# Kernel tuning notes

Hardware: AMD Instinct MI355X
Metric: run time of the kernel (lower is better)

Reference implementation:

```python
import jax, jax.numpy as jnp
import numpy as np

B, T = 128, 50
VOCAB, EMB_D, GRU_H = 10000, 200, 100
HEADS, AHID, THID = 8, 96, 96

def _conv(x, w, b, pad):
    y = jax.lax.conv_general_dilated(x, w, (1, 1), pad,
        dimension_numbers=('NCHW', 'OIHW', 'NCHW'))
    return y + b[None, :, None, None]

def _bn(x, g, b, m, v):
    s = jax.lax.rsqrt(v + 1e-5)
    return (x - m[None, :, None, None]) * (g * s)[None, :, None, None] + b[None, :, None, None]

def _maxpool(x):
    return jax.lax.reduce_window(x, -jnp.inf, jax.lax.max, (1, 1, 2, 2), (1, 1, 2, 2), 'VALID')

def _resize(x):
    # F.interpolate(mode='bilinear', align_corners=False) == half-pixel bilinear, no antialias
    return jax.image.resize(x, (x.shape[0], x.shape[1], 25, 156), 'bilinear', antialias=False)

def _audio_attn(x, wq, bq, wk, bk, wv, bv):
    # x: [B,96,H,W]; wq: [heads,96,96] == stacked per-head 1x1 convs
    Q = jnp.einsum('bchw,noc->bnohw', x, wq) + bq[None, :, :, None, None]
    K = jnp.einsum('bchw,noc->bnohw', x, wk) + bk[None, :, :, None, None]
    V = jnp.einsum('bchw,noc->bnohw', x, wv) + bv[None, :, :, None, None]
    # torch F.softmax with no dim on a 4D tensor defaults to dim=1 (channels) -> axis=2 here
    return jax.nn.softmax(Q * K, axis=2) * V  # [B,heads,96,H,W]

def _text_attn(o, wq, bq, wk, bk, wv, bv):
    # o: [N,100]; wq: [heads,96,100] == stacked per-head Linear layers
    Q = jnp.einsum('nd,hod->nho', o, wq) + bq[None]
    K = jnp.einsum('nd,hod->nho', o, wk) + bk[None]
    V = jnp.einsum('nd,hod->nho', o, wv) + bv[None]
    a = jax.nn.softmax(Q * K, axis=2) * V  # 2D softmax default dim=1 -> over feature axis
    return a.reshape(o.shape[0], -1)  # head-concat order == torch cat along dim=1

def _gru(xs, w_ih, w_hh, b_ih, b_hh):
    # xs: [T,B,200]; torch gate order r, z, n; b_hn applied inside r-gating
    def step(h, x):
        gi = x @ w_ih.T + b_ih
        gh = h @ w_hh.T + b_hh
        ir, iz, inew = jnp.split(gi, 3, axis=1)
        hr, hz, hnew = jnp.split(gh, 3, axis=1)
        r = jax.nn.sigmoid(ir + hr)
        z = jax.nn.sigmoid(iz + hz)
        n = jnp.tanh(inew + r * hnew)
        h2 = (1.0 - z) * n + z * h
        return h2, h2
    h0 = jnp.zeros((xs.shape[1], GRU_H), xs.dtype)
    hT, outs = jax.lax.scan(step, h0, xs)
    return outs, hT

def _forward(tokens, lengths, mfcc_t, mfcc_f, mfcc_c, w1a, b1a, g1a, be1a, m1a, v1a, w1b, b1b, g1b, be1b, m1b, v1b, w2, b2, g2, be2, m2, v2, w3, b3, g3, be3, m3, v3, w4, b4, g4, be4, m4, v4, wq_a1, bq_a1, wk_a1, bk_a1, wv_a1, bv_a1, wq_a2, bq_a2, wk_a2, bk_a2, wv_a2, bv_a2, emb, w_ih, w_hh, b_ih, b_hh, wq_t1, bq_t1, wk_t1, bk_t1, wv_t1, bv_t1, wq_t2, bq_t2, wk_t2, bk_t2, wv_t2, bv_t2, w_fa, b_fa, w_ft, b_ft, w_e, b_e):
    # --- audio CNN stem (eval-mode batchnorm; dropout off) ---
    xa = jax.nn.relu(_bn(_conv(mfcc_t, w1a, b1a, 'VALID'), g1a, be1a, m1a, v1a))
    xb = jax.nn.relu(_bn(_conv(mfcc_f, w1b, b1b, 'VALID'), g1b, be1b, m1b, v1b))
    # NOTE: original source reuses conv1b/bn1b for the third input (faithful to that)
    xc = jax.nn.relu(_bn(_conv(mfcc_c, w1b, b1b, 'VALID'), g1b, be1b, m1b, v1b))
    x = jnp.concatenate([_resize(xa), _resize(xb), _resize(xc)], axis=1)  # [B,24,25,156]
    x = _maxpool(jax.nn.relu(_bn(_conv(x, w2, b2, [(1, 1), (1, 1)]), g2, be2, m2, v2)))  # [B,32,12,78]
    x = _maxpool(jax.nn.relu(_bn(_conv(x, w3, b3, [(1, 1), (1, 1)]), g3, be3, m3, v3)))  # [B,64,6,39]
    x = jax.nn.relu(_bn(_conv(x, w4, b4, [(1, 1), (1, 1)]), g4, be4, m4, v4))            # [B,96,6,39]
    # --- two stacked per-head audio attentions, then per-head spatial GAP ---
    a1 = _audio_attn(x, wq_a1, bq_a1, wk_a1, bk_a1, wv_a1, bv_a1).mean(axis=(-2, -1))  # [B,8,96]
    a2 = _audio_attn(x, wq_a2, bq_a2, wk_a2, bk_a2, wv_a2, bv_a2).mean(axis=(-2, -1))
    # forward() slices heads along the height concat and GAPs -> per head [stage1 96, stage2 96]
    self_attn_audio = jnp.concatenate([a1, a2], axis=2).reshape(x.shape[0], -1)  # [B,1536]
    # --- text branch: embedding + GRU (all lengths == T -> pack/pad is identity) ---
    ex = jnp.swapaxes(emb[tokens], 0, 1)  # [T,B,200]
    outs, h = _gru(ex, w_ih, w_hh, b_ih, b_hh)  # h: [B,100]
    output = jnp.swapaxes(outs, 0, 1).reshape(-1, GRU_H)  # [B*T,100]
    t1 = _text_attn(output, wq_t1, bq_t1, wk_t1, bk_t1, wv_t1, bv_t1)
    t2 = _text_attn(output, wq_t2, bq_t2, wk_t2, bk_t2, wv_t2, bv_t2)
    self_attn_text = jnp.concatenate([t1, t2], axis=1).reshape(x.shape[0], T, -1).sum(axis=1)  # [B,1536]
    # --- cross-modal gated fusion ---
    x_gap = x.mean(axis=(-2, -1))  # [B,96]
    a_text = jax.nn.softmax(x_gap @ w_fa.T + b_fa, axis=1)   # [B,100]
    attn_text_based_audio = a_text * h                        # [B,100]
    a_audio = jax.nn.softmax(h @ w_ft.T + b_ft, axis=1)      # [B,96]
    attn_audio_based_text = a_audio * x_gap                   # [B,96]
    feat = jnp.concatenate([self_attn_audio, self_attn_text,
                            attn_audio_based_text, attn_text_based_audio], axis=1)  # [B,3268]
    return feat @ w_e.T + b_e  # [B,4] emotion logits

def setup_inputs() -> dict:
    key = jax.random.key(0)
    ks = iter(jax.random.split(key, 100))
    nrm = lambda s, sc=0.05: jax.random.normal(next(ks), s, jnp.float32) * sc
    uni = lambda s: jax.random.uniform(next(ks), s, jnp.float32) * 0.5 + 0.5
    d = {}
    d['mfcc_t'] = jax.random.normal(next(ks), (B, 1, 200, 40), jnp.float32)
    d['mfcc_f'] = jax.random.normal(next(ks), (B, 1, 200, 40), jnp.float32)
    d['mfcc_c'] = jax.random.normal(next(ks), (B, 1, 200, 40), jnp.float32)
    d['tokens'] = jax.random.randint(next(ks), (B, T), 0, VOCAB)
    d['lengths'] = jnp.full((B,), T, jnp.int32)
    def bnp(pre, c):
        d['g' + pre] = 1.0 + nrm((c,)); d['be' + pre] = nrm((c,))
        d['m' + pre] = nrm((c,)); d['v' + pre] = uni((c,))
    d['w1a'] = nrm((8, 1, 5, 2), 0.2); d['b1a'] = nrm((8,)); bnp('1a', 8)
    d['w1b'] = nrm((8, 1, 2, 6), 0.2); d['b1b'] = nrm((8,)); bnp('1b', 8)
    d['w2'] = nrm((32, 24, 3, 3), 0.1); d['b2'] = nrm((32,)); bnp('2', 32)
    d['w3'] = nrm((64, 32, 3, 3), 0.1); d['b3'] = nrm((64,)); bnp('3', 64)
    d['w4'] = nrm((96, 64, 3, 3), 0.08); d['b4'] = nrm((96,)); bnp('4', 96)
    for s in ('1', '2'):
        for p in ('q', 'k', 'v'):
            d['w%s_a%s' % (p, s)] = nrm((HEADS, 96, 96), 0.1)
            d['b%s_a%s' % (p, s)] = nrm((HEADS, 96))
    d['emb'] = nrm((VOCAB, EMB_D), 0.1)
    d['w_ih'] = nrm((3 * GRU_H, EMB_D), 0.1); d['w_hh'] = nrm((3 * GRU_H, GRU_H), 0.1)
    d['b_ih'] = nrm((3 * GRU_H,)); d['b_hh'] = nrm((3 * GRU_H,))
    for s in ('1', '2'):
        for p in ('q', 'k', 'v'):
            d['w%s_t%s' % (p, s)] = nrm((HEADS, THID, GRU_H), 0.1)
            d['b%s_t%s' % (p, s)] = nrm((HEADS, THID))
    d['w_fa'] = nrm((100, 96), 0.1); d['b_fa'] = nrm((100,))
    d['w_ft'] = nrm((96, 100), 0.1); d['b_ft'] = nrm((96,))
    d['w_e'] = nrm((4, 2 * HEADS * AHID + 2 * HEADS * THID + 96 + 100), 0.05); d['b_e'] = nrm((4,))
    return d

def reference(mfcc_t, mfcc_f, mfcc_c, tokens, lengths, w1a, b1a, g1a, be1a, m1a, v1a, w1b, b1b, g1b, be1b, m1b, v1b, w2, b2, g2, be2, m2, v2, w3, b3, g3, be3, m3, v3, w4, b4, g4, be4, m4, v4, wq_a1, bq_a1, wk_a1, bk_a1, wv_a1, bv_a1, wq_a2, bq_a2, wk_a2, bk_a2, wv_a2, bv_a2, emb, w_ih, w_hh, b_ih, b_hh, wq_t1, bq_t1, wk_t1, bk_t1, wv_t1, bv_t1, wq_t2, bq_t2, wk_t2, bk_t2, wv_t2, bv_t2, w_fa, b_fa, w_ft, b_ft, w_e, b_e):
    return _forward(tokens, lengths, mfcc_t, mfcc_f, mfcc_c, w1a, b1a, g1a, be1a, m1a, v1a, w1b, b1b, g1b, be1b, m1b, v1b, w2, b2, g2, be2, m2, v2, w3, b3, g3, be3, m3, v3, w4, b4, g4, be4, m4, v4, wq_a1, bq_a1, wk_a1, bk_a1, wv_a1, bv_a1, wq_a2, bq_a2, wk_a2, bk_a2, wv_a2, bv_a2, emb, w_ih, w_hh, b_ih, b_hh, wq_t1, bq_t1, wk_t1, bk_t1, wv_t1, bv_t1, wq_t2, bq_t2, wk_t2, bk_t2, wv_t2, bv_t2, w_fa, b_fa, w_ft, b_ft, w_e, b_e)
```

## Files before the change

kernel.cpp:

```cpp
#include <hip/hip_runtime.h>
#include <math.h>

static constexpr int kB = 128;
static constexpr int kT = 50;

struct TDesc { const float* src; float* dst; int O; int C; int total; };
struct TPack { TDesc d[15]; };
__global__ void k_transpose_pack(TPack p, float* __restrict__ za) {
    if (blockIdx.y == 15) {
        for (int i = blockIdx.x * 256 + threadIdx.x; i < 196608; i += 76800)
            za[i] = 0.f;
        return;
    }
    TDesc t = p.d[blockIdx.y];
    int idx = blockIdx.x * 256 + threadIdx.x;
    if (idx >= t.total) return;
    int o = idx % t.O; int r = idx / t.O; int c = r % t.C; int n = r / t.C;
    t.dst[idx] = t.src[((size_t)n * t.O + o) * t.C + c];
}

__global__ void __launch_bounds__(320) k_gi(const int* __restrict__ tokens,
        const float* __restrict__ emb, const float* __restrict__ w_ih,
        const float* __restrict__ b_ih, float* __restrict__ GI) {
    int r0 = blockIdx.x * 8;
    int tid = threadIdx.x;
    __shared__ float er[8][200];
    for (int e = tid; e < 1600; e += 320) {
        int r = e / 200, c = e - r * 200;
        er[r][c] = emb[(size_t)tokens[r0 + r] * 200 + c];
    }
    __syncthreads();
    if (tid < 300) {
        float acc[8];
        float bv = b_ih[tid];
        #pragma unroll
        for (int r = 0; r < 8; ++r) acc[r] = bv;
        for (int k4 = 0; k4 < 50; ++k4) {
            float4 w4 = *(const float4*)(w_ih + (size_t)tid * 200 + k4 * 4);
            #pragma unroll
            for (int r = 0; r < 8; ++r) {
                float4 x4 = *(const float4*)&er[r][k4 * 4];
                acc[r] += w4.x * x4.x + w4.y * x4.y + w4.z * x4.z + w4.w * x4.w;
            }
        }
        #pragma unroll
        for (int r = 0; r < 8; ++r)
            GI[(size_t)(r0 + r) * 300 + tid] = acc[r];
    }
}

__global__ void __launch_bounds__(256) k_fat_stem_gru(
    const float* __restrict__ mt, const float* __restrict__ mf,
    const float* __restrict__ mc,
    const float* __restrict__ w1a, const float* __restrict__ b1a,
    const float* __restrict__ g1a, const float* __restrict__ be1a,
    const float* __restrict__ m1a, const float* __restrict__ v1a,
    const float* __restrict__ w1b, const float* __restrict__ b1b,
    const float* __restrict__ g1b, const float* __restrict__ be1b,
    const float* __restrict__ m1b, const float* __restrict__ v1b,
    float* __restrict__ out, int total,
    const float* __restrict__ GI, const float* __restrict__ w_hh,
    const float* __restrict__ b_hh, float* __restrict__ outs) {
    if (blockIdx.x < 128) {
        const int b = blockIdx.x, tid = threadIdx.x;
        __shared__ float hs[100];
        __shared__ float gH[300];
        const float bias0 = b_hh[tid];
        const float bias1 = (tid < 44) ? b_hh[256 + tid] : 0.f;
        if (tid < 100) hs[tid] = 0.f;
        __syncthreads();
        for (int t = 0; t < kT; ++t) {
            {
                float gh = bias0;
                const float* wr = w_hh + (size_t)tid * 100;
                #pragma unroll
                for (int k4 = 0; k4 < 25; ++k4) {
                    float4 w4 = *(const float4*)(wr + k4 * 4);
                    float4 h4 = *(const float4*)&hs[k4 * 4];
                    gh += w4.x * h4.x + w4.y * h4.y + w4.z * h4.z + w4.w * h4.w;
                }
                gH[tid] = gh;
            }
            if (tid < 44) {
                float gh = bias1;
                const float* wr = w_hh + (size_t)(256 + tid) * 100;
                #pragma unroll
                for (int k4 = 0; k4 < 25; ++k4) {
                    float4 w4 = *(const float4*)(wr + k4 * 4);
                    float4 h4 = *(const float4*)&hs[k4 * 4];
                    gh += w4.x * h4.x + w4.y * h4.y + w4.z * h4.z + w4.w * h4.w;
                }
                gH[256 + tid] = gh;
            }
            __syncthreads();
            if (tid < 100) {
                const float* gi = GI + ((size_t)b * kT + t) * 300;
                float r = 1.f / (1.f + expf(-(gi[tid] + gH[tid])));
                float z = 1.f / (1.f + expf(-(gi[100 + tid] + gH[100 + tid])));
                float nn = tanhf(gi[200 + tid] + r * gH[200 + tid]);
                float h2 = (1.f - z) * nn + z * hs[tid];
                hs[tid] = h2;
                outs[((size_t)b * kT + t) * 100 + tid] = h2;
            }
            __syncthreads();
        }
        return;
    }
    int idx = (blockIdx.x - 128) * 256 + threadIdx.x;
    if (idx >= total) return;
    int ox = idx % 156; int t = idx / 156;
    int oy = t % 25; t /= 25;
    int ch = t % 24; int b = t / 24;
    int grp = ch >> 3, c = ch & 7;
    const float* src; int Hc, Wc;
    const float *wb, *cb, *g, *be, *m, *v;
    if (grp == 0) { src = mt; Hc = 196; Wc = 39; wb = w1a + c * 10;
                    cb = b1a; g = g1a; be = be1a; m = m1a; v = v1a; }
    else          { src = (grp == 1 ? mf : mc); Hc = 199; Wc = 35; wb = w1b + c * 12;
                    cb = b1b; g = g1b; be = be1b; m = m1b; v = v1b; }
    float s = g[c] * rsqrtf(v[c] + 1e-5f);
    float bias = (cb[c] - m[c]) * s + be[c];
    float sy = (oy + 0.5f) * ((float)Hc / 25.f) - 0.5f;
    float sx = (ox + 0.5f) * ((float)Wc / 156.f) - 0.5f;
    float fy0 = floorf(sy), fx0 = floorf(sx);
    float fy = sy - fy0, fx = sx - fx0;
    int y0 = (int)fy0, x0 = (int)fx0;
    int y0c = min(max(y0, 0), Hc - 1), y1c = min(max(y0 + 1, 0), Hc - 1);
    int x0c = min(max(x0, 0), Wc - 1), x1c = min(max(x0 + 1, 0), Wc - 1);
    bool xs = (x1c == x0c), ys = (y1c == y0c);
    const float* p = src + (size_t)b * 8000;
    float t00, t01, t10, t11;
    if (grp == 0) {
        float W[6][3];
        #pragma unroll
        for (int r = 0; r < 6; ++r) {
            int rr = min(y0c + r, 199);
            #pragma unroll
            for (int cc = 0; cc < 3; ++cc)
                W[r][cc] = p[rr * 40 + min(x0c + cc, 39)];
        }
        float a00 = 0.f, a01 = 0.f, a10 = 0.f, a11 = 0.f;
        #pragma unroll
        for (int ky = 0; ky < 5; ++ky)
            #pragma unroll
            for (int kx = 0; kx < 2; ++kx) {
                float wv = wb[ky * 2 + kx];
                a00 += W[ky][kx] * wv;     a01 += W[ky][kx + 1] * wv;
                a10 += W[ky + 1][kx] * wv; a11 += W[ky + 1][kx + 1] * wv;
            }
        t00 = a00;
        t01 = xs ? a00 : a01;
        t10 = ys ? a00 : a10;
        t11 = xs ? (ys ? a00 : a10) : (ys ? a01 : a11);
    } else {
        float W[3][7];
        #pragma unroll
        for (int r = 0; r < 3; ++r) {
            int rr = min(y0c + r, 199);
            #pragma unroll
            for (int cc = 0; cc < 7; ++cc)
                W[r][cc] = p[rr * 40 + min(x0c + cc, 39)];
        }
        float a00 = 0.f, a01 = 0.f, a10 = 0.f, a11 = 0.f;
        #pragma unroll
        for (int ky = 0; ky < 2; ++ky)
            #pragma unroll
            for (int kx = 0; kx < 6; ++kx) {
                float wv = wb[ky * 6 + kx];
                a00 += W[ky][kx] * wv;     a01 += W[ky][kx + 1] * wv;
                a10 += W[ky + 1][kx] * wv; a11 += W[ky + 1][kx + 1] * wv;
            }
        t00 = a00;
        t01 = xs ? a00 : a01;
        t10 = ys ? a00 : a10;
        t11 = xs ? (ys ? a00 : a10) : (ys ? a01 : a11);
    }
    float r00 = fmaxf(t00 * s + bias, 0.f), r01 = fmaxf(t01 * s + bias, 0.f);
    float r10 = fmaxf(t10 * s + bias, 0.f), r11 = fmaxf(t11 * s + bias, 0.f);
    out[idx] = r00 * (1.f - fy) * (1.f - fx) + r01 * (1.f - fy) * fx
             + r10 * fy * (1.f - fx) + r11 * fy * fx;
}

template<int CIN, int CI_T, int H, int W, int ROWS, int NPX>
__global__ void __launch_bounds__(256) k_conv3x3_tiled(
    const float* __restrict__ in, const float* __restrict__ wT,
    const float* __restrict__ cb, const float* __restrict__ g,
    const float* __restrict__ be, const float* __restrict__ m,
    const float* __restrict__ v, float* __restrict__ out, int COUT) {
    constexpr int WP = W + 2;
    constexpr int RP = ROWS + 2;
    constexpr int STAGE = CI_T * RP * WP;
    __shared__ float sx[STAGE];
    __shared__ float sw[CI_T * 9 * 8];
    const int b = blockIdx.x, rt = blockIdx.y, oc0 = blockIdx.z * 8;
    const int row0 = rt * ROWS;
    const int tid = threadIdx.x;

    int off[NPX]; bool val[NPX];
    #pragma unroll
    for (int j = 0; j < NPX; ++j) {
        int px = tid + j * 256;
        int oy = px / W, ox = px - oy * W;
        bool ok = (px < ROWS * W) && (row0 + oy < H);
        val[j] = ok;
        off[j] = ok ? (oy * WP + ox) : 0;
    }

    float acc[NPX][8];
    #pragma unroll
    for (int j = 0; j < NPX; ++j)
        #pragma unroll
        for (int o = 0; o < 8; ++o) acc[j][o] = 0.f;

    for (int c0 = 0; c0 < CIN; c0 += CI_T) {
        __syncthreads();
        for (int e = tid; e < STAGE; e += 256) {
            int ci = e / (RP * WP);
            int rem = e - ci * RP * WP;
            int r = rem / WP;
            int xx = rem - r * WP;
            int iy = row0 - 1 + r;
            int ix = xx - 1;
            float vv = 0.f;
            if (iy >= 0 && iy < H && ix >= 0 && ix < W)
                vv = in[((size_t)(b * CIN + c0 + ci) * H + iy) * W + ix];
            sx[e] = vv;
        }
        for (int e = tid; e < CI_T * 9 * 8; e += 256) {
            int rk = e >> 3;
            int o = e & 7;
            sw[e] = wT[((size_t)c0 * 9 + rk) * COUT + oc0 + o];
        }
        __syncthreads();
        #pragma unroll 1
        for (int cl = 0; cl < CI_T; ++cl) {
            const float* sxc = sx + cl * RP * WP;
            #pragma unroll
            for (int k = 0; k < 9; ++k) {
                const int ky = k / 3, kx = k % 3;
                const float4 wa = *(const float4*)(sw + (cl * 9 + k) * 8);
                const float4 wb = *(const float4*)(sw + (cl * 9 + k) * 8 + 4);
                #pragma unroll
                for (int j = 0; j < NPX; ++j) {
                    float xv = sxc[off[j] + ky * WP + kx];
                    acc[j][0] += xv * wa.x; acc[j][1] += xv * wa.y;
                    acc[j][2] += xv * wa.z; acc[j][3] += xv * wa.w;
                    acc[j][4] += xv * wb.x; acc[j][5] += xv * wb.y;
                    acc[j][6] += xv * wb.z; acc[j][7] += xv * wb.w;
                }
            }
        }
    }
    float sc[8], bi[8];
    #pragma unroll
    for (int o = 0; o < 8; ++o) {
        float s = g[oc0 + o] * rsqrtf(v[oc0 + o] + 1e-5f);
        sc[o] = s; bi[o] = (cb[oc0 + o] - m[oc0 + o]) * s + be[oc0 + o];
    }
    #pragma unroll
    for (int j = 0; j < NPX; ++j) if (val[j]) {
        int px = tid + j * 256;
        int oy = row0 + px / W, ox = px % W;
        #pragma unroll
        for (int o = 0; o < 8; ++o)
            out[((size_t)(b * COUT + oc0 + o) * H + oy) * W + ox] =
                fmaxf(acc[j][o] * sc[o] + bi[o], 0.f);
    }
}

__global__ void k_maxpool(const float* __restrict__ in, float* __restrict__ out,
                          int C, int Hin, int Win, int Hout, int Wout, int total) {
    int idx = blockIdx.x * blockDim.x + threadIdx.x;
    if (idx >= total) return;
    int ox = idx % Wout; int t = idx / Wout;
    int oy = t % Hout; t /= Hout;
    int c = t % C; int b = t / C;
    const float* p = in + ((size_t)(b * C + c) * Hin + 2 * oy) * Win + 2 * ox;
    float m0 = fmaxf(p[0], p[1]);
    float m1 = fmaxf(p[Win], p[Win + 1]);
    out[idx] = fmaxf(m0, m1);
}

__global__ void __launch_bounds__(256) k_xgap(const float* __restrict__ x,
                                              float* __restrict__ xgap) {
    int b = blockIdx.x, tid = threadIdx.x;
    int wave = tid >> 6, lane = tid & 63;
    for (int c = wave; c < 96; c += 4) {
        const float* row = x + ((size_t)b * 96 + c) * 234;
        float s = 0.f;
        for (int p = lane; p < 234; p += 64) s += row[p];
        #pragma unroll
        for (int off = 1; off < 64; off <<= 1) s += __shfl_xor(s, off);
        if (lane == 0) xgap[b * 96 + c] = s * (1.f / 234.f);
    }
}

__global__ void __launch_bounds__(256, 2) k_audio_attn(
    const float* __restrict__ x,
    const float* __restrict__ wq1, const float* __restrict__ bq1,
    const float* __restrict__ wk1, const float* __restrict__ bk1,
    const float* __restrict__ wv1, const float* __restrict__ bv1,
    const float* __restrict__ wq2, const float* __restrict__ bq2,
    const float* __restrict__ wk2, const float* __restrict__ bk2,
    const float* __restrict__ wv2, const float* __restrict__ bv2,
    float* __restrict__ afeat) {
    const int b = blockIdx.x >> 1, pt = blockIdx.x & 1;
    const int n = blockIdx.y, stage = blockIdx.z;
    const float* wq = (stage ? wq2 : wq1) + n * 9216;
    const float* wk = (stage ? wk2 : wk1) + n * 9216;
    const float* wv = (stage ? wv2 : wv1) + n * 9216;
    const float* bqn = (stage ? bq2 : bq1) + n * 96;
    const float* bkn = (stage ? bk2 : bk1) + n * 96;
    const float* bvn = (stage ? bv2 : bv1) + n * 96;
    const int tid = threadIdx.x;
    const int to = tid >> 4, tpg = tid & 15;
    const int ob = to * 6;
    const int pA = tpg * 4;
    const int p0 = pt * 128;

    __shared__ float sxc[16 * 128];
    __shared__ float sw[4608];
    float* sred = sw;

    const float* xb = x + (size_t)b * (96 * 234) + p0;

    float qa[6][8], ka[6][8], va[6][8];
    #pragma unroll
    for (int j = 0; j < 6; ++j) {
        float bq_ = bqn[ob + j], bk_ = bkn[ob + j], bv_ = bvn[ob + j];
        #pragma unroll
        for (int i = 0; i < 8; ++i) { qa[j][i] = bq_; ka[j][i] = bk_; va[j][i] = bv_; }
    }

    for (int c0 = 0; c0 < 96; c0 += 16) {
        __syncthreads();
        {
            #pragma unroll
            for (int it = 0; it < 4; ++it) {
                int e2 = tid + it * 256;
                int r = e2 >> 6, c2 = (e2 & 63) * 2;
                float2 v = make_float2(0.f, 0.f);
                if (p0 + c2 < 234) v = *(const float2*)(xb + (c0 + r) * 234 + c2);
                *(float2*)(sxc + r * 128 + c2) = v;
            }
        }
        for (int e4 = tid; e4 < 1152; e4 += 256) {
            int mat = (e4 >= 768) ? 2 : (e4 >= 384 ? 1 : 0);
            int r4 = e4 - mat * 384;
            const float* wsrc = (mat == 0) ? wq : (mat == 1 ? wk : wv);
            *(float4*)(sw + mat * 1536 + r4 * 4) = *(const float4*)(wsrc + c0 * 96 + r4 * 4);
        }
        __syncthreads();
        #pragma unroll 2
        for (int cc = 0; cc < 16; ++cc) {
            float4 xa = *(const float4*)(sxc + cc * 128 + pA);
            float4 xc = *(const float4*)(sxc + cc * 128 + 64 + pA);
            const float* wr = sw + cc * 96 + ob;
            float2 q01 = *(const float2*)(wr);
            float2 q23 = *(const float2*)(wr + 2);
            float2 q45 = *(const float2*)(wr + 4);
            float2 k01 = *(const float2*)(wr + 1536);
            float2 k23 = *(const float2*)(wr + 1538);
            float2 k45 = *(const float2*)(wr + 1540);
            float2 v01 = *(const float2*)(wr + 3072);
            float2 v23 = *(const float2*)(wr + 3074);
            float2 v45 = *(const float2*)(wr + 3076);
            float wqv[6] = {q01.x, q01.y, q23.x, q23.y, q45.x, q45.y};
            float wkv[6] = {k01.x, k01.y, k23.x, k23.y, k45.x, k45.y};
            float wvv[6] = {v01.x, v01.y, v23.x, v23.y, v45.x, v45.y};
            #pragma unroll
            for (int j = 0; j < 6; ++j) {
                qa[j][0] += wqv[j] * xa.x; qa[j][1] += wqv[j] * xa.y;
                qa[j][2] += wqv[j] * xa.z; qa[j][3] += wqv[j] * xa.w;
                qa[j][4] += wqv[j] * xc.x; qa[j][5] += wqv[j] * xc.y;
                qa[j][6] += wqv[j] * xc.z; qa[j][7] += wqv[j] * xc.w;
                ka[j][0] += wkv[j] * xa.x; ka[j][1] += wkv[j] * xa.y;
                ka[j][2] += wkv[j] * xa.z; ka[j][3] += wkv[j] * xa.w;
                ka[j][4] += wkv[j] * xc.x; ka[j][5] += wkv[j] * xc.y;
                ka[j][6] += wkv[j] * xc.z; ka[j][7] += wkv[j] * xc.w;
                va[j][0] += wvv[j] * xa.x; va[j][1] += wvv[j] * xa.y;
                va[j][2] += wvv[j] * xa.z; va[j][3] += wvv[j] * xa.w;
                va[j][4] += wvv[j] * xc.x; va[j][5] += wvv[j] * xc.y;
                va[j][6] += wvv[j] * xc.z; va[j][7] += wvv[j] * xc.w;
            }
        }
    }

    int col[8];
    #pragma unroll
    for (int i = 0; i < 4; ++i) { col[i] = pA + i; col[4 + i] = 64 + pA + i; }

    float pmx[8];
    #pragma unroll
    for (int i = 0; i < 8; ++i) pmx[i] = -1e30f;
    #pragma unroll
    for (int j = 0; j < 6; ++j)
        #pragma unroll
        for (int i = 0; i < 8; ++i) {
            float sv = qa[j][i] * ka[j][i];
            qa[j][i] = sv;
            pmx[i] = fmaxf(pmx[i], sv);
        }
    __syncthreads();
    #pragma unroll
    for (int i = 0; i < 8; ++i) sred[to * 128 + col[i]] = pmx[i];
    __syncthreads();
    float m_[8];
    #pragma unroll
    for (int i = 0; i < 8; ++i) {
        float mm = -1e30f;
        for (int t = 0; t < 16; ++t) mm = fmaxf(mm, sred[t * 128 + col[i]]);
        m_[i] = mm;
    }
    __syncthreads();
    float z[8];
    #pragma unroll
    for (int i = 0; i < 8; ++i) z[i] = 0.f;
    #pragma unroll
    for (int j = 0; j < 6; ++j)
        #pragma unroll
        for (int i = 0; i < 8; ++i) {
            float e = __expf(qa[j][i] - m_[i]);
            qa[j][i] = e;
            z[i] += e;
        }
    #pragma unroll
    for (int i = 0; i < 8; ++i) sred[to * 128 + col[i]] = z[i];
    __syncthreads();
    float rz[8];
    #pragma unroll
    for (int i = 0; i < 8; ++i) {
        float zs = 0.f;
        for (int t = 0; t < 16; ++t) zs += sred[t * 128 + col[i]];
        rz[i] = (p0 + col[i] < 234) ? 1.f / zs : 0.f;
    }
    __syncthreads();
    #pragma unroll
    for (int j = 0; j < 6; ++j) {
        float po = 0.f;
        #pragma unroll
        for (int i = 0; i < 8; ++i) po += qa[j][i] * rz[i] * va[j][i];
        sred[(ob + j) * 16 + tpg] = po;
    }
    __syncthreads();
    if (tid < 96) {
        float ssum = 0.f;
        #pragma unroll
        for (int t = 0; t < 16; ++t) ssum += sred[tid * 16 + t];
        atomicAdd(afeat + b * 1536 + n * 192 + stage * 96 + tid, ssum * (1.f / 234.f));
    }
}

__global__ void __launch_bounds__(128) k_text_attn(const float* __restrict__ outs,
    const float* __restrict__ wq1, const float* __restrict__ bq1,
    const float* __restrict__ wk1, const float* __restrict__ bk1,
    const float* __restrict__ wv1, const float* __restrict__ bv1,
    const float* __restrict__ wq2, const float* __restrict__ bq2,
    const float* __restrict__ wk2, const float* __restrict__ bk2,
    const float* __restrict__ wv2, const float* __restrict__ bv2,
    float* __restrict__ tfeat) {
    int b = blockIdx.x, stage = blockIdx.y, n = blockIdx.z;
    const float* wq = stage ? wq2 : wq1; const float* bq = stage ? bq2 : bq1;
    const float* wk = stage ? wk2 : wk1; const float* bk = stage ? bk2 : bk1;
    const float* wv = stage ? wv2 : wv1; const float* bv = stage ? bv2 : bv1;
    int tid = threadIdx.x;
    bool act = tid < 96;
    int oo = act ? tid : 0;
    const float* wqc = wq + n * 9600 + oo;
    const float* wkc = wk + n * 9600 + oo;
    const float* wvc = wv + n * 9600 + oo;
    float bqv = act ? bq[n * 96 + tid] : 0.f;
    float bkv = act ? bk[n * 96 + tid] : 0.f;
    float bvv = act ? bv[n * 96 + tid] : 0.f;
    __shared__ float rows[10][100];
    __shared__ float wredM[2][10], wredS[2][10];
    float acc = 0.f;
    int wave = tid >> 6, lane = tid & 63;
    for (int tile = 0; tile < 5; ++tile) {
        int t0 = tile * 10;
        __syncthreads();
        for (int e = tid; e < 1000; e += 128) {
            int tt = e / 100, c = e - tt * 100;
            rows[tt][c] = outs[((size_t)b * kT + t0 + tt) * 100 + c];
        }
        __syncthreads();
        float q[10], k[10], v[10];
        #pragma unroll
        for (int tt = 0; tt < 10; ++tt) { q[tt] = bqv; k[tt] = bkv; v[tt] = bvv; }
        for (int c4 = 0; c4 < 25; ++c4) {
            int cb = c4 * 4 * 96;
            float q0 = wqc[cb], q1 = wqc[cb + 96], q2 = wqc[cb + 192], q3 = wqc[cb + 288];
            float k0 = wkc[cb], k1 = wkc[cb + 96], k2 = wkc[cb + 192], k3 = wkc[cb + 288];
            float v0 = wvc[cb], v1 = wvc[cb + 96], v2 = wvc[cb + 192], v3 = wvc[cb + 288];
            #pragma unroll
            for (int tt = 0; tt < 10; ++tt) {
                float4 x4 = *(const float4*)&rows[tt][c4 * 4];
                q[tt] += q0 * x4.x + q1 * x4.y + q2 * x4.z + q3 * x4.w;
                k[tt] += k0 * x4.x + k1 * x4.y + k2 * x4.z + k3 * x4.w;
                v[tt] += v0 * x4.x + v1 * x4.y + v2 * x4.z + v3 * x4.w;
            }
        }
        float s[10], e_[10];
        #pragma unroll
        for (int tt = 0; tt < 10; ++tt) s[tt] = act ? q[tt] * k[tt] : -1e30f;
        #pragma unroll
        for (int tt = 0; tt < 10; ++tt) {
            float m = s[tt];
            #pragma unroll
            for (int off = 1; off < 64; off <<= 1) m = fmaxf(m, __shfl_xor(m, off));
            if (lane == 0) wredM[wave][tt] = m;
        }
        __syncthreads();
        #pragma unroll
        for (int tt = 0; tt < 10; ++tt) {
            float mx = fmaxf(wredM[0][tt], wredM[1][tt]);
            e_[tt] = expf(s[tt] - mx);
        }
        #pragma unroll
        for (int tt = 0; tt < 10; ++tt) {
            float sm = e_[tt];
            #pragma unroll
            for (int off = 1; off < 64; off <<= 1) sm += __shfl_xor(sm, off);
            if (lane == 0) wredS[wave][tt] = sm;
        }
        __syncthreads();
        #pragma unroll
        for (int tt = 0; tt < 10; ++tt) {
            float sm = wredS[0][tt] + wredS[1][tt];
            acc += e_[tt] / sm * v[tt];
        }
    }
    if (act) tfeat[b * 1536 + stage * 768 + n * 96 + tid] = acc;
}

__global__ void __launch_bounds__(128) k_final(const float* __restrict__ xgap,
    const float* __restrict__ outs, const float* __restrict__ afeat,
    const float* __restrict__ tfeat,
    const float* __restrict__ w_fa, const float* __restrict__ b_fa,
    const float* __restrict__ w_ft, const float* __restrict__ b_ft,
    const float* __restrict__ w_e, const float* __restrict__ b_e,
    float* __restrict__ out) {
    int b = blockIdx.x; int tid = threadIdx.x;
    __shared__ float xg[96], hv[100], st[100], sa[96], aat[96], atba[100];
    __shared__ float redm[2], reds[2];
    if (tid < 96) xg[tid] = xgap[b * 96 + tid];
    if (tid < 100) hv[tid] = outs[(size_t)(b * kT + kT - 1) * 100 + tid];
    __syncthreads();
    if (tid < 100) {
        float acc = b_fa[tid];
        const float* wr = w_fa + tid * 96;
        for (int c = 0; c < 96; ++c) acc += wr[c] * xg[c];
        st[tid] = acc;
    }
    if (tid < 96) {
        float acc = b_ft[tid];
        const float* wr = w_ft + tid * 100;
        for (int c = 0; c < 100; ++c) acc += wr[c] * hv[c];
        sa[tid] = acc;
    }
    __syncthreads();
    if (tid == 0) {
        float mxv = -1e30f; for (int i = 0; i < 100; ++i) mxv = fmaxf(mxv, st[i]);
        float s = 0.f; for (int i = 0; i < 100; ++i) s += expf(st[i] - mxv);
        redm[0] = mxv; reds[0] = s;
    }
    if (tid == 1) {
        float mxv = -1e30f; for (int i = 0; i < 96; ++i) mxv = fmaxf(mxv, sa[i]);
        float s = 0.f; for (int i = 0; i < 96; ++i) s += expf(sa[i] - mxv);
        redm[1] = mxv; reds[1] = s;
    }
    __syncthreads();
    if (tid < 100) atba[tid] = expf(st[tid] - redm[0]) / reds[0] * hv[tid];
    if (tid < 96)  aat[tid]  = expf(sa[tid] - redm[1]) / reds[1] * xg[tid];
    __syncthreads();
    float a0 = 0.f, a1 = 0.f, a2 = 0.f, a3 = 0.f;
    for (int col = tid; col < 3268; col += 128) {
        float f;
        if (col < 1536)      f = afeat[b * 1536 + col];
        else if (col < 3072) f = tfeat[b * 1536 + col - 1536];
        else if (col < 3168) f = aat[col - 3072];
        else                 f = atba[col - 3168];
        a0 += w_e[col] * f;            a1 += w_e[3268 + col] * f;
        a2 += w_e[2 * 3268 + col] * f; a3 += w_e[3 * 3268 + col] * f;
    }
    __shared__ float r4[4][128];
    r4[0][tid] = a0; r4[1][tid] = a1; r4[2][tid] = a2; r4[3][tid] = a3;
    __syncthreads();
    if (tid < 4) {
        float s = 0.f;
        for (int i = 0; i < 128; ++i) s += r4[tid][i];
        out[b * 4 + tid] = s + b_e[tid];
    }
}

extern "C" void kernel_launch(void* const* d_in, const int* in_sizes, int n_in,
                              void* d_out, int out_size, void* d_ws, size_t ws_size,
                              hipStream_t stream) {
    (void)in_sizes; (void)n_in; (void)out_size; (void)ws_size;
    const float* mfcc_t = (const float*)d_in[0];
    const float* mfcc_f = (const float*)d_in[1];
    const float* mfcc_c = (const float*)d_in[2];
    const int*   tokens = (const int*)d_in[3];
    const float *w1a = (const float*)d_in[5],  *b1a = (const float*)d_in[6],
                *g1a = (const float*)d_in[7],  *be1a = (const float*)d_in[8],
                *m1a = (const float*)d_in[9],  *v1a = (const float*)d_in[10];
    const float *w1b = (const float*)d_in[11], *b1b = (const float*)d_in[12],
                *g1b = (const float*)d_in[13], *be1b = (const float*)d_in[14],
                *m1b = (const float*)d_in[15], *v1b = (const float*)d_in[16];
    const float *w2 = (const float*)d_in[17], *b2 = (const float*)d_in[18],
                *g2 = (const float*)d_in[19], *be2 = (const float*)d_in[20],
                *m2 = (const float*)d_in[21], *v2 = (const float*)d_in[22];
    const float *w3 = (const float*)d_in[23], *b3 = (const float*)d_in[24],
                *g3 = (const float*)d_in[25], *be3 = (const float*)d_in[26],
                *m3 = (const float*)d_in[27], *v3 = (const float*)d_in[28];
    const float *w4 = (const float*)d_in[29], *b4 = (const float*)d_in[30],
                *g4 = (const float*)d_in[31], *be4 = (const float*)d_in[32],
                *m4 = (const float*)d_in[33], *v4 = (const float*)d_in[34];
    const float *wq_a1 = (const float*)d_in[35], *bq_a1 = (const float*)d_in[36],
                *wk_a1 = (const float*)d_in[37], *bk_a1 = (const float*)d_in[38],
                *wv_a1 = (const float*)d_in[39], *bv_a1 = (const float*)d_in[40];
    const float *wq_a2 = (const float*)d_in[41], *bq_a2 = (const float*)d_in[42],
                *wk_a2 = (const float*)d_in[43], *bk_a2 = (const float*)d_in[44],
                *wv_a2 = (const float*)d_in[45], *bv_a2 = (const float*)d_in[46];
    const float *emb  = (const float*)d_in[47];
    const float *w_ih = (const float*)d_in[48], *w_hh = (const float*)d_in[49],
                *b_ih = (const float*)d_in[50], *b_hh = (const float*)d_in[51];
    const float *wq_t1 = (const float*)d_in[52], *bq_t1 = (const float*)d_in[53],
                *wk_t1 = (const float*)d_in[54], *bk_t1 = (const float*)d_in[55],
                *wv_t1 = (const float*)d_in[56], *bv_t1 = (const float*)d_in[57];
    const float *wq_t2 = (const float*)d_in[58], *bq_t2 = (const float*)d_in[59],
                *wk_t2 = (const float*)d_in[60], *bk_t2 = (const float*)d_in[61],
                *wv_t2 = (const float*)d_in[62], *bv_t2 = (const float*)d_in[63];
    const float *w_fa = (const float*)d_in[64], *b_fa = (const float*)d_in[65],
                *w_ft = (const float*)d_in[66], *b_ft = (const float*)d_in[67],
                *w_e  = (const float*)d_in[68], *b_e  = (const float*)d_in[69];

    float* ws = (float*)d_ws;
    const size_t Z0 = 0;
    const size_t Z1 = 22091776ull;
    const size_t OUTS  = 34072576ull;
    const size_t AFEAT = 34712576ull;
    const size_t TFEAT = 34909184ull;
    const size_t XGAP  = 35105792ull;
    const size_t WT    = 35118080ull;
    float* GI = ws + Z0;
    float* X1 = ws + Z1;
    float* C2 = ws + Z0;  float* P2 = ws + Z1;
    float* C3 = ws + Z0;  float* P3 = ws + Z1;
    float* X4 = ws + Z0;
    float* outs  = ws + OUTS;
    float* afeat = ws + AFEAT;
    float* tfeat = ws + TFEAT;
    float* xgap  = ws + XGAP;
    float* wqa1t = ws + WT;
    float* wka1t = wqa1t + 73728; float* wva1t = wka1t + 73728;
    float* wqa2t = wva1t + 73728; float* wka2t = wqa2t + 73728; float* wva2t = wka2t + 73728;
    float* wqt1t = wva2t + 73728;
    float* wkt1t = wqt1t + 76800; float* wvt1t = wkt1t + 76800;
    float* wqt2t = wvt1t + 76800; float* wkt2t = wqt2t + 76800; float* wvt2t = wkt2t + 76800;
    float* wT2 = tfeat;
    float* wT3 = tfeat + 6912;
    float* wT4 = tfeat + 25344;

    TPack tp;
    tp.d[0]  = {wq_a1, wqa1t, 96, 96, 73728};
    tp.d[1]  = {wk_a1, wka1t, 96, 96, 73728};
    tp.d[2]  = {wv_a1, wva1t, 96, 96, 73728};
    tp.d[3]  = {wq_a2, wqa2t, 96, 96, 73728};
    tp.d[4]  = {wk_a2, wka2t, 96, 96, 73728};
    tp.d[5]  = {wv_a2, wva2t, 96, 96, 73728};
    tp.d[6]  = {w2, wT2, 32, 216, 6912};
    tp.d[7]  = {w3, wT3, 64, 288, 18432};
    tp.d[8]  = {w4, wT4, 96, 576, 55296};
    tp.d[9]  = {wq_t1, wqt1t, 96, 100, 76800};
    tp.d[10] = {wk_t1, wkt1t, 96, 100, 76800};
    tp.d[11] = {wv_t1, wvt1t, 96, 100, 76800};
    tp.d[12] = {wq_t2, wqt2t, 96, 100, 76800};
    tp.d[13] = {wk_t2, wkt2t, 96, 100, 76800};
    tp.d[14] = {wv_t2, wvt2t, 96, 100, 76800};
    k_transpose_pack<<<dim3(300, 16), 256, 0, stream>>>(tp, afeat);

    k_gi<<<kB * kT / 8, 320, 0, stream>>>(tokens, emb, w_ih, b_ih, GI);

    k_fat_stem_gru<<<46928, 256, 0, stream>>>(mfcc_t, mfcc_f, mfcc_c,
        w1a, b1a, g1a, be1a, m1a, v1a,
        w1b, b1b, g1b, be1b, m1b, v1b, X1, 11980800,
        GI, w_hh, b_hh, outs);

    k_conv3x3_tiled<24, 8, 25, 156, 9, 6><<<dim3(128, 3, 4), 256, 0, stream>>>(
        X1, wT2, b2, g2, be2, m2, v2, C2, 32);
    k_maxpool<<<14976, 256, 0, stream>>>(C2, P2, 32, 25, 156, 12, 78, 3833856);
    k_conv3x3_tiled<32, 8, 12, 78, 12, 4><<<dim3(128, 1, 8), 256, 0, stream>>>(
        P2, wT3, b3, g3, be3, m3, v3, C3, 64);
    k_maxpool<<<7488, 256, 0, stream>>>(C3, P3, 64, 12, 78, 6, 39, 1916928);
    k_conv3x3_tiled<64, 16, 6, 39, 6, 1><<<dim3(128, 1, 12), 256, 0, stream>>>(
        P3, wT4, b4, g4, be4, m4, v4, X4, 96);

    k_text_attn<<<dim3(kB, 2, 8), 128, 0, stream>>>(outs,
        wqt1t, bq_t1, wkt1t, bk_t1, wvt1t, bv_t1,
        wqt2t, bq_t2, wkt2t, bk_t2, wvt2t, bv_t2, tfeat);
    k_xgap<<<kB, 256, 0, stream>>>(X4, xgap);

    k_audio_attn<<<dim3(kB * 2, 8, 2), 256, 0, stream>>>(X4,
        wqa1t, bq_a1, wka1t, bk_a1, wva1t, bv_a1,
        wqa2t, bq_a2, wka2t, bk_a2, wva2t, bv_a2, afeat);

    k_final<<<kB, 128, 0, stream>>>(xgap, outs, afeat, tfeat,
                                    w_fa, b_fa, w_ft, b_ft, w_e, b_e, (float*)d_out);
}
```

Baseline: 1.419 ms.

## Retile text attention with register-blocked QKV projection and transposed GRU output

```diff
diff --git a/kernel.cpp b/kernel.cpp
--- a/kernel.cpp
+++ b/kernel.cpp
@@ -60,7 +60,7 @@
     const float* __restrict__ m1b, const float* __restrict__ v1b,
     float* __restrict__ out, int total,
     const float* __restrict__ GI, const float* __restrict__ w_hh,
-    const float* __restrict__ b_hh, float* __restrict__ outs) {
+    const float* __restrict__ b_hh, float* __restrict__ outsT) {
     if (blockIdx.x < 128) {
         const int b = blockIdx.x, tid = threadIdx.x;
         __shared__ float hs[100];
@@ -100,7 +100,7 @@
                 float nn = tanhf(gi[200 + tid] + r * gH[200 + tid]);
                 float h2 = (1.f - z) * nn + z * hs[tid];
                 hs[tid] = h2;
-                outs[((size_t)b * kT + t) * 100 + tid] = h2;
+                outsT[((size_t)b * 100 + tid) * kT + t] = h2;
             }
             __syncthreads();
         }
@@ -451,7 +451,8 @@
     }
 }
 
-__global__ void __launch_bounds__(128) k_text_attn(const float* __restrict__ outs,
+__global__ void __launch_bounds__(256, 2) k_text_attn(
+    const float* __restrict__ outsT,
     const float* __restrict__ wq1, const float* __restrict__ bq1,
     const float* __restrict__ wk1, const float* __restrict__ bk1,
     const float* __restrict__ wv1, const float* __restrict__ bv1,
@@ -459,82 +460,133 @@
     const float* __restrict__ wk2, const float* __restrict__ bk2,
     const float* __restrict__ wv2, const float* __restrict__ bv2,
     float* __restrict__ tfeat) {
-    int b = blockIdx.x, stage = blockIdx.y, n = blockIdx.z;
-    const float* wq = stage ? wq2 : wq1; const float* bq = stage ? bq2 : bq1;
-    const float* wk = stage ? wk2 : wk1; const float* bk = stage ? bk2 : bk1;
-    const float* wv = stage ? wv2 : wv1; const float* bv = stage ? bv2 : bv1;
-    int tid = threadIdx.x;
-    bool act = tid < 96;
-    int oo = act ? tid : 0;
-    const float* wqc = wq + n * 9600 + oo;
-    const float* wkc = wk + n * 9600 + oo;
-    const float* wvc = wv + n * 9600 + oo;
-    float bqv = act ? bq[n * 96 + tid] : 0.f;
-    float bkv = act ? bk[n * 96 + tid] : 0.f;
-    float bvv = act ? bv[n * 96 + tid] : 0.f;
-    __shared__ float rows[10][100];
-    __shared__ float wredM[2][10], wredS[2][10];
-    float acc = 0.f;
-    int wave = tid >> 6, lane = tid & 63;
-    for (int tile = 0; tile < 5; ++tile) {
-        int t0 = tile * 10;
+    const int b = blockIdx.x, stage = blockIdx.y, n = blockIdx.z;
+    const float* wq = (stage ? wq2 : wq1) + n * 9600;
+    const float* wk = (stage ? wk2 : wk1) + n * 9600;
+    const float* wv = (stage ? wv2 : wv1) + n * 9600;
+    const float* bqn = (stage ? bq2 : bq1) + n * 96;
+    const float* bkn = (stage ? bk2 : bk1) + n * 96;
+    const float* bvn = (stage ? bv2 : bv1) + n * 96;
+    const int tid = threadIdx.x;
+    const int to = tid >> 4, tpg = tid & 15;
+    const int ob = to * 6;
+    const int tA = tpg * 4;
+
+    __shared__ float sxc[20 * 64];
+    __shared__ float sw[5760];
+    float* sred = sw;
+
+    const float* xb = outsT + (size_t)b * (100 * kT);
+
+    float qa[6][4], ka[6][4], va[6][4];
+    #pragma unroll
+    for (int j = 0; j < 6; ++j) {
+        float bq_ = bqn[ob + j], bk_ = bkn[ob + j], bv_ = bvn[ob + j];
+        #pragma unroll
+        for (int i = 0; i < 4; ++i) { qa[j][i] = bq_; ka[j][i] = bk_; va[j][i] = bv_; }
+    }
+
+    for (int c0 = 0; c0 < 100; c0 += 20) {
         __syncthreads();
-        for (int e = tid; e < 1000; e += 128) {
-            int tt = e / 100, c = e - tt * 100;
-            rows[tt][c] = outs[((size_t)b * kT + t0 + tt) * 100 + c];
+        for (int e = tid; e < 1280; e += 256) {
+            int r = e >> 6, tt = e & 63;
+            sxc[e] = (tt < kT) ? xb[(c0 + r) * kT + tt] : 0.f;
+        }
+        for (int e4 = tid; e4 < 1440; e4 += 256) {
+            int mat = (e4 >= 960) ? 2 : (e4 >= 480 ? 1 : 0);
+            int r4 = e4 - mat * 480;
+            const float* wsrc = (mat == 0) ? wq : (mat == 1 ? wk : wv);
+            *(float4*)(sw + mat * 1920 + r4 * 4) = *(const float4*)(wsrc + c0 * 96 + r4 * 4);
         }
         __syncthreads();
-        float q[10], k[10], v[10];
-        #pragma unroll
-        for (int tt = 0; tt < 10; ++tt) { q[tt] = bqv; k[tt] = bkv; v[tt] = bvv; }
-        for (int c4 = 0; c4 < 25; ++c4) {
-            int cb = c4 * 4 * 96;
-            float q0 = wqc[cb], q1 = wqc[cb + 96], q2 = wqc[cb + 192], q3 = wqc[cb + 288];
-            float k0 = wkc[cb], k1 = wkc[cb + 96], k2 = wkc[cb + 192], k3 = wkc[cb + 288];
-            float v0 = wvc[cb], v1 = wvc[cb + 96], v2 = wvc[cb + 192], v3 = wvc[cb + 288];
-            #pragma unroll
-            for (int tt = 0; tt < 10; ++tt) {
-                float4 x4 = *(const float4*)&rows[tt][c4 * 4];
-                q[tt] += q0 * x4.x + q1 * x4.y + q2 * x4.z + q3 * x4.w;
-                k[tt] += k0 * x4.x + k1 * x4.y + k2 * x4.z + k3 * x4.w;
-                v[tt] += v0 * x4.x + v1 * x4.y + v2 * x4.z + v3 * x4.w;
-            }
-        }
-        float s[10], e_[10];
-        #pragma unroll
-        for (int tt = 0; tt < 10; ++tt) s[tt] = act ? q[tt] * k[tt] : -1e30f;
-        #pragma unroll
-        for (int tt = 0; tt < 10; ++tt) {
-            float m = s[tt];
-            #pragma unroll
-            for (int off = 1; off < 64; off <<= 1) m = fmaxf(m, __shfl_xor(m, off));
-            if (lane == 0) wredM[wave][tt] = m;
-        }
-        __syncthreads();
-        #pragma unroll
-        for (int tt = 0; tt < 10; ++tt) {
-            float mx = fmaxf(wredM[0][tt], wredM[1][tt]);
-            e_[tt] = expf(s[tt] - mx);
-        }
-        #pragma unroll
-        for (int tt = 0; tt < 10; ++tt) {
-            float sm = e_[tt];
-            #pragma unroll
-            for (int off = 1; off < 64; off <<= 1) sm += __shfl_xor(sm, off);
-            if (lane == 0) wredS[wave][tt] = sm;
-        }
-        __syncthreads();
-        #pragma unroll
-        for (int tt = 0; tt < 10; ++tt) {
-            float sm = wredS[0][tt] + wredS[1][tt];
-            acc += e_[tt] / sm * v[tt];
-        }
-    }
-    if (act) tfeat[b * 1536 + stage * 768 + n * 96 + tid] = acc;
+        #pragma unroll 4
+        for (int cc = 0; cc < 20; ++cc) {
+            float4 xa = *(const float4*)(sxc + cc * 64 + tA);
+            const float* wr = sw + cc * 96 + ob;
+            float2 q01 = *(const float2*)(wr);
+            float2 q23 = *(const float2*)(wr + 2);
+            float2 q45 = *(const float2*)(wr + 4);
+            float2 k01 = *(const float2*)(wr + 1920);
+            float2 k23 = *(const float2*)(wr + 1922);
+            float2 k45 = *(const float2*)(wr + 1924);
+            float2 v01 = *(const float2*)(wr + 3840);
+            float2 v23 = *(const float2*)(wr + 3842);
+            float2 v45 = *(const float2*)(wr + 3844);
+            float wqv[6] = {q01.x, q01.y, q23.x, q23.y, q45.x, q45.y};
+            float wkv[6] = {k01.x, k01.y, k23.x, k23.y, k45.x, k45.y};
+            float wvv[6] = {v01.x, v01.y, v23.x, v23.y, v45.x, v45.y};
+            #pragma unroll
+            for (int j = 0; j < 6; ++j) {
+                qa[j][0] += wqv[j] * xa.x; qa[j][1] += wqv[j] * xa.y;
+                qa[j][2] += wqv[j] * xa.z; qa[j][3] += wqv[j] * xa.w;
+                ka[j][0] += wkv[j] * xa.x; ka[j][1] += wkv[j] * xa.y;
+                ka[j][2] += wkv[j] * xa.z; ka[j][3] += wkv[j] * xa.w;
+                va[j][0] += wvv[j] * xa.x; va[j][1] += wvv[j] * xa.y;
+                va[j][2] += wvv[j] * xa.z; va[j][3] += wvv[j] * xa.w;
+            }
+        }
+    }
+
+    float pmx[4] = {-1e30f, -1e30f, -1e30f, -1e30f};
+    #pragma unroll
+    for (int j = 0; j < 6; ++j)
+        #pragma unroll
+        for (int i = 0; i < 4; ++i) {
+            float sv = qa[j][i] * ka[j][i];
+            qa[j][i] = sv;
+            pmx[i] = fmaxf(pmx[i], sv);
+        }
+    __syncthreads();
+    #pragma unroll
+    for (int i = 0; i < 4; ++i) sred[to * 64 + tA + i] = pmx[i];
+    __syncthreads();
+    float m_[4];
+    #pragma unroll
+    for (int i = 0; i < 4; ++i) {
+        float mm = -1e30f;
+        for (int t = 0; t < 16; ++t) mm = fmaxf(mm, sred[t * 64 + tA + i]);
+        m_[i] = mm;
+    }
+    __syncthreads();
+    float z[4] = {0.f, 0.f, 0.f, 0.f};
+    #pragma unroll
+    for (int j = 0; j < 6; ++j)
+        #pragma unroll
+        for (int i = 0; i < 4; ++i) {
+            float e = __expf(qa[j][i] - m_[i]);
+            qa[j][i] = e;
+            z[i] += e;
+        }
+    #pragma unroll
+    for (int i = 0; i < 4; ++i) sred[to * 64 + tA + i] = z[i];
+    __syncthreads();
+    float rz[4];
+    #pragma unroll
+    for (int i = 0; i < 4; ++i) {
+        float zs = 0.f;
+        for (int t = 0; t < 16; ++t) zs += sred[t * 64 + tA + i];
+        rz[i] = (tA + i < kT) ? 1.f / zs : 0.f;
+    }
+    __syncthreads();
+    #pragma unroll
+    for (int j = 0; j < 6; ++j) {
+        float po = qa[j][0] * rz[0] * va[j][0]
+                 + qa[j][1] * rz[1] * va[j][1]
+                 + qa[j][2] * rz[2] * va[j][2]
+                 + qa[j][3] * rz[3] * va[j][3];
+        sred[(ob + j) * 16 + tpg] = po;
+    }
+    __syncthreads();
+    if (tid < 96) {
+        float ssum = 0.f;
+        #pragma unroll
+        for (int t = 0; t < 16; ++t) ssum += sred[tid * 16 + t];
+        tfeat[b * 1536 + stage * 768 + n * 96 + tid] = ssum;
+    }
 }
 
 __global__ void __launch_bounds__(128) k_final(const float* __restrict__ xgap,
-    const float* __restrict__ outs, const float* __restrict__ afeat,
+    const float* __restrict__ outsT, const float* __restrict__ afeat,
     const float* __restrict__ tfeat,
     const float* __restrict__ w_fa, const float* __restrict__ b_fa,
     const float* __restrict__ w_ft, const float* __restrict__ b_ft,
@@ -544,7 +596,7 @@
     __shared__ float xg[96], hv[100], st[100], sa[96], aat[96], atba[100];
     __shared__ float redm[2], reds[2];
     if (tid < 96) xg[tid] = xgap[b * 96 + tid];
-    if (tid < 100) hv[tid] = outs[(size_t)(b * kT + kT - 1) * 100 + tid];
+    if (tid < 100) hv[tid] = outsT[((size_t)b * 100 + tid) * kT + (kT - 1)];
     __syncthreads();
     if (tid < 100) {
         float acc = b_fa[tid];
@@ -648,7 +700,7 @@
     float* C2 = ws + Z0;  float* P2 = ws + Z1;
     float* C3 = ws + Z0;  float* P3 = ws + Z1;
     float* X4 = ws + Z0;
-    float* outs  = ws + OUTS;
+    float* outsT = ws + OUTS;
     float* afeat = ws + AFEAT;
     float* tfeat = ws + TFEAT;
     float* xgap  = ws + XGAP;
@@ -685,7 +737,7 @@
     k_fat_stem_gru<<<46928, 256, 0, stream>>>(mfcc_t, mfcc_f, mfcc_c,
         w1a, b1a, g1a, be1a, m1a, v1a,
         w1b, b1b, g1b, be1b, m1b, v1b, X1, 11980800,
-        GI, w_hh, b_hh, outs);
+        GI, w_hh, b_hh, outsT);
 
     k_conv3x3_tiled<24, 8, 25, 156, 9, 6><<<dim3(128, 3, 4), 256, 0, stream>>>(
         X1, wT2, b2, g2, be2, m2, v2, C2, 32);
@@ -696,7 +748,7 @@
     k_conv3x3_tiled<64, 16, 6, 39, 6, 1><<<dim3(128, 1, 12), 256, 0, stream>>>(
         P3, wT4, b4, g4, be4, m4, v4, X4, 96);
 
-    k_text_attn<<<dim3(kB, 2, 8), 128, 0, stream>>>(outs,
+    k_text_attn<<<dim3(kB, 2, 8), 256, 0, stream>>>(outsT,
         wqt1t, bq_t1, wkt1t, bk_t1, wvt1t, bv_t1,
         wqt2t, bq_t2, wkt2t, bk_t2, wvt2t, bv_t2, tfeat);
     k_xgap<<<kB, 256, 0, stream>>>(X4, xgap);
@@ -705,6 +757,6 @@
         wqa1t, bq_a1, wka1t, bk_a1, wva1t, bv_a1,
         wqa2t, bq_a2, wka2t, bk_a2, wva2t, bv_a2, afeat);
 
-    k_final<<<kB, 128, 0, stream>>>(xgap, outs, afeat, tfeat,
+    k_final<<<kB, 128, 0, stream>>>(xgap, outsT, afeat, tfeat,
                                     w_fa, b_fa, w_ft, b_ft, w_e, b_e, (float*)d_out);
 }
```

New measurement: 1.346 ms. 1.05x faster.
